# Kernel optimization log

Hardware: AMD Instinct MI355X
Metric: run time of the kernel (lower is better)

The kernel has to match this reference:

```python
import jax, jax.numpy as jnp
import numpy as np

B, LAGS, POOL, D, H, NTS = 16, 4096, 4, 512, 8, 1000
S = LAGS // POOL          # num_pools = 1024
DH = D // H               # head dim = 64


def _layernorm_dim1(x, gamma, beta, eps=1e-5):
    # torch code: mean/var over dim=1 (channel axis), unbiased var, per-position affine
    mean = jnp.mean(x, axis=1, keepdims=True)
    var = jnp.var(x, axis=1, keepdims=True, ddof=1)
    unit = (x - mean) / jnp.sqrt(eps + var)
    return gamma * unit + beta


def setup_inputs() -> dict:
    key = jax.random.key(0)
    ks = jax.random.split(key, 16)
    inp = {
        "ts": jax.random.normal(ks[0], (B, 1, LAGS), dtype=jnp.float32),
        "te": jax.random.randint(ks[1], (B, 1), 0, NTS),
        "conv_w": jax.random.normal(ks[2], (D, 1, POOL), dtype=jnp.float32) * (1.0 / POOL) ** 0.5,
        "conv_b": jax.random.normal(ks[3], (D,), dtype=jnp.float32) * 0.02,
        "pe_emb": jax.random.normal(ks[4], (S, D), dtype=jnp.float32),
        "ts_emb": jax.random.normal(ks[5], (NTS, D), dtype=jnp.float32),
        "ln1_g": jnp.ones((S,), dtype=jnp.float32),
        "ln1_b": jnp.zeros((S,), dtype=jnp.float32),
        "dense_M": jax.random.normal(ks[6], (D, D), dtype=jnp.float32) * D ** -0.5,
        "Wq": jax.random.normal(ks[7], (H, DH, D), dtype=jnp.float32) * D ** -0.5,
        "Wk": jax.random.normal(ks[8], (H, DH, D), dtype=jnp.float32) * D ** -0.5,
        "Wv": jax.random.normal(ks[9], (H, DH, D), dtype=jnp.float32) * D ** -0.5,
        "Wo": jax.random.normal(ks[10], (D, D), dtype=jnp.float32) * D ** -0.5,
        "bo": jnp.zeros((D, 1), dtype=jnp.float32),
        "ln2_g": jnp.ones((S,), dtype=jnp.float32),
        "ln2_b": jnp.zeros((S,), dtype=jnp.float32),
    }
    return inp


def _forward(ts, te, conv_w, conv_b, pe_emb, ts_emb, ln1_g, ln1_b,
             dense_M, Wq, Wk, Wv, Wo, bo, ln2_g, ln2_b):
    # Conv1d with stride == kernel_size: non-overlapping patches
    xr = ts.reshape(B, S, POOL)                                   # (B,S,P)
    conv = jnp.einsum('bsp,dp->bds', xr, conv_w[:, 0, :]) + conv_b[:, None]  # (B,D,S)
    conv = conv + pe_emb.T                                        # positional add (D,S)
    act = jax.nn.gelu(conv, approximate=False)
    n1 = _layernorm_dim1(act, ln1_g, ln1_b)
    dense = jnp.einsum('ed,bds->bes', dense_M, n1)                # Linear: M @ x
    dense = dense + ts_emb[te[:, 0]][:, :, None]                  # ts embedding (B,D,1)

    # multi-head attention, Q=K=V=dense; vectorized over heads
    Qd = jnp.einsum('hcd,bds->bhcs', Wq, dense)                   # (B,H,DH,S)
    Kd = jnp.einsum('hcd,bds->bhcs', Wk, dense)
    Vd = jnp.einsum('hcd,bds->bhcs', Wv, dense)
    scores = jnp.einsum('bhci,bhcj->bhij', Qd, Kd) / DH ** 0.5    # (B,H,S,S)
    i_idx = jnp.arange(S)
    mask = i_idx[:, None] > i_idx[None, :]                        # tril(diagonal=-1): i>j -> -inf
    scores = jnp.where(mask, -jnp.inf, scores)
    sm = jax.nn.softmax(scores, axis=2)                           # softmax over dim 1 of (S,S)
    attn = jnp.einsum('bhci,bhij->bhcj', Vd, sm)                  # V @ softmaxed
    cat = attn.reshape(B, D, S)                                   # concat heads on dim 1
    out = jnp.einsum('ed,bds->bes', Wo, cat) + bo[None]           # final linear + bias
    res = out + conv                                              # residual
    return _layernorm_dim1(res, ln2_g, ln2_b)


def reference(ts, te, conv_w, conv_b, pe_emb, ts_emb, ln1_g, ln1_b,
              dense_M, Wq, Wk, Wv, Wo, bo, ln2_g, ln2_b):
    return _forward(ts, te, conv_w, conv_b, pe_emb, ts_emb, ln1_g, ln1_b,
                    dense_M, Wq, Wk, Wv, Wo, bo, ln2_g, ln2_b)
```

## Files before the change

kernel.cpp:

```cpp
#include <hip/hip_runtime.h>
#include <hip/hip_bf16.h>

#define B_ 16
#define S_ 1024
#define D_ 512
#define H_ 8
#define DH_ 64

typedef __attribute__((ext_vector_type(8))) short bf16x8;
typedef __attribute__((ext_vector_type(4))) short bf16x4;
typedef __attribute__((ext_vector_type(4))) float f32x4;
typedef __attribute__((ext_vector_type(16))) float f32x16;

__device__ __forceinline__ short f2bf(float f) {
    __hip_bfloat16 h = __float2bfloat16(f);
    return *reinterpret_cast<short*>(&h);
}
__device__ __forceinline__ unsigned pack_bf2(float lo, float hi) {
    unsigned a = (unsigned)(unsigned short)f2bf(lo);
    unsigned b = (unsigned)(unsigned short)f2bf(hi);
    return a | (b << 16);
}
__device__ __forceinline__ void gload16(const void* g, void* l) {
    __builtin_amdgcn_global_load_lds(
        (const __attribute__((address_space(1))) unsigned int*)g,
        (__attribute__((address_space(3))) unsigned int*)l, 16, 0, 0);
}

__global__ __launch_bounds__(256) void prep_w(
    const float* __restrict__ M, const float* __restrict__ Wq,
    const float* __restrict__ Wk, const float* __restrict__ Wv,
    const float* __restrict__ Wo, __hip_bfloat16* __restrict__ wb)
{
    const int gid = blockIdx.x * 256 + threadIdx.x;
    const int e8 = gid * 8;
    const int w = e8 >> 18;
    const int off = e8 & 262143;
    const float* src = (w == 0) ? M : (w == 1) ? Wq : (w == 2) ? Wk
                      : (w == 3) ? Wv : Wo;
    const float scale = (w == 1) ? 0.18033688011112042f : 1.0f;
    const float4 f0 = *reinterpret_cast<const float4*>(src + off);
    const float4 f1 = *reinterpret_cast<const float4*>(src + off + 4);
    union { short s[8]; bf16x8 v; } r;
    r.s[0] = f2bf(f0.x * scale); r.s[1] = f2bf(f0.y * scale);
    r.s[2] = f2bf(f0.z * scale); r.s[3] = f2bf(f0.w * scale);
    r.s[4] = f2bf(f1.x * scale); r.s[5] = f2bf(f1.y * scale);
    r.s[6] = f2bf(f1.z * scale); r.s[7] = f2bf(f1.w * scale);
    *reinterpret_cast<bf16x8*>(wb + e8) = r.v;
}

__global__ __launch_bounds__(256) void k1_conv_gelu_ln(
    const float* __restrict__ ts, const float* __restrict__ conv_w,
    const float* __restrict__ conv_b, const float* __restrict__ pe,
    const float* __restrict__ g1, const float* __restrict__ b1,
    __hip_bfloat16* __restrict__ n1)
{
    const int w = threadIdx.x >> 6, lane = threadIdx.x & 63;
    const int row = blockIdx.x * 4 + w;
    const int b = row >> 10, s = row & 1023;
    const float4 x = *reinterpret_cast<const float4*>(ts + b * 4096 + s * 4);
    const int d0 = lane * 8;

    const float4 cb0 = *reinterpret_cast<const float4*>(conv_b + d0);
    const float4 cb1 = *reinterpret_cast<const float4*>(conv_b + d0 + 4);
    const float4 pe0 = *reinterpret_cast<const float4*>(pe + s * 512 + d0);
    const float4 pe1 = *reinterpret_cast<const float4*>(pe + s * 512 + d0 + 4);
    const float cbv[8] = {cb0.x, cb0.y, cb0.z, cb0.w, cb1.x, cb1.y, cb1.z, cb1.w};
    const float pev[8] = {pe0.x, pe0.y, pe0.z, pe0.w, pe1.x, pe1.y, pe1.z, pe1.w};

    float a[8];
    float sum = 0.f, sq = 0.f;
#pragma unroll
    for (int j = 0; j < 8; ++j) {
        const float4 wv = *reinterpret_cast<const float4*>(conv_w + (d0 + j) * 4);
        float v = x.x * wv.x + x.y * wv.y + x.z * wv.z + x.w * wv.w
                + cbv[j] + pev[j];
        v = 0.5f * v * (1.0f + erff(v * 0.70710678118654752f));
        a[j] = v; sum += v; sq += v * v;
    }
#pragma unroll
    for (int off = 1; off < 64; off <<= 1) {
        sum += __shfl_xor(sum, off);
        sq  += __shfl_xor(sq, off);
    }
    const float mean = sum * (1.0f / 512.0f);
    const float var  = (sq - 512.0f * mean * mean) * (1.0f / 511.0f);
    const float rstd = rsqrtf(var + 1e-5f);
    const float gg = g1[s], bb = b1[s];
    union { short sh[8]; bf16x8 v; } o;
#pragma unroll
    for (int j = 0; j < 8; ++j)
        o.sh[j] = f2bf(gg * ((a[j] - mean) * rstd) + bb);
    *reinterpret_cast<bf16x8*>(n1 + (size_t)row * 512 + d0) = o.v;
}

template<int MODE>
__global__ __launch_bounds__(256) void gemm_k(
    const __hip_bfloat16* __restrict__ A,
    const __hip_bfloat16* __restrict__ Wb,
    void* __restrict__ outp,
    const float* __restrict__ aux,
    const int* __restrict__ te)
{
    __shared__ char lA[128 * 128];
    __shared__ char lB[128 * 128];

    const int t = threadIdx.x;
    const int lane = t & 63;
    const int w = t >> 6;
    const int wm = w & 1, wn = w >> 1;
    const int Rb = blockIdx.x * 128;
    const int Nb = blockIdx.y * 128;
    const int g = lane >> 4, lr = lane & 15;
    const int lrow = lane >> 3;
    const int coff = ((lane & 7) ^ lrow) * 8;

    f32x4 acc[4][4];
#pragma unroll
    for (int i = 0; i < 4; ++i)
#pragma unroll
        for (int j = 0; j < 4; ++j) acc[i][j] = {0.f, 0.f, 0.f, 0.f};

    for (int kt = 0; kt < 8; ++kt) {
        const int k0 = kt * 64;
#pragma unroll
        for (int i = 0; i < 4; ++i) {
            const int r0 = w * 32 + i * 8;
            gload16(A + (size_t)(Rb + r0 + lrow) * 512 + k0 + coff, lA + r0 * 128);
        }
#pragma unroll
        for (int i = 0; i < 4; ++i) {
            const int r0 = w * 32 + i * 8;
            gload16(Wb + (size_t)(Nb + r0 + lrow) * 512 + k0 + coff, lB + r0 * 128);
        }
        __syncthreads();
#pragma unroll
        for (int kk = 0; kk < 2; ++kk) {
            bf16x8 af[4], bfv[4];
            const int ch = kk * 4 + g;
#pragma unroll
            for (int mt = 0; mt < 4; ++mt) {
                const int row = wm * 64 + mt * 16 + lr;
                af[mt] = *reinterpret_cast<const bf16x8*>(
                    lA + row * 128 + ((ch ^ (row & 7)) << 4));
            }
#pragma unroll
            for (int nt = 0; nt < 4; ++nt) {
                const int row = wn * 64 + nt * 16 + lr;
                bfv[nt] = *reinterpret_cast<const bf16x8*>(
                    lB + row * 128 + ((ch ^ (row & 7)) << 4));
            }
#pragma unroll
            for (int mt = 0; mt < 4; ++mt)
#pragma unroll
                for (int nt = 0; nt < 4; ++nt)
                    acc[mt][nt] = __builtin_amdgcn_mfma_f32_16x16x32_bf16(
                        af[mt], bfv[nt], acc[mt][nt], 0, 0, 0);
        }
        __syncthreads();
    }

#pragma unroll
    for (int mt = 0; mt < 4; ++mt) {
#pragma unroll
        for (int nt = 0; nt < 4; ++nt) {
#pragma unroll
            for (int r = 0; r < 4; ++r) {
                const int R = Rb + wm * 64 + mt * 16 + 4 * g + r;
                const int N = Nb + wn * 64 + nt * 16 + lr;
                float v = acc[mt][nt][r];
                if (MODE == 0) {
                    const int b = R >> 10;
                    v += aux[(size_t)te[b] * 512 + N];
                    reinterpret_cast<__hip_bfloat16*>(outp)[(size_t)R * 512 + N] =
                        __float2bfloat16(v);
                } else if (MODE == 1) {
                    const int b = R >> 10, s = R & 1023, h = N >> 6, c = N & 63;
                    reinterpret_cast<__hip_bfloat16*>(outp)
                        [(((size_t)(b * 8 + h)) * 1024 + s) * 64 + c] = __float2bfloat16(v);
                } else if (MODE == 2) {
                    const int b = R >> 10, s = R & 1023, h = N >> 6, c = N & 63;
                    reinterpret_cast<__hip_bfloat16*>(outp)
                        [(((size_t)(b * 8 + h)) * 64 + c) * 1024 + s] = __float2bfloat16(v);
                } else {
                    reinterpret_cast<float*>(outp)[(size_t)R * 512 + N] = v + aux[N];
                }
            }
        }
    }
}

__device__ __forceinline__ void write_strip(
    __hip_bfloat16* __restrict__ dstbase, const int jw0,
    const f32x16& o0, const f32x16& o1, const float lsum,
    const int l5, const int ln31)
{
    const float linv = 1.0f / lsum;
#pragma unroll
    for (int r = 0; r < 16; ++r) {
        const int jrow = (r & 3) + 8 * (r >> 2) + 4 * l5;
        const float rinv = __shfl(linv, jrow);
        __hip_bfloat16* dst = dstbase + (size_t)(jw0 + jrow) * 512;
        dst[ln31]      = __float2bfloat16(o0[r] * rinv);
        dst[32 + ln31] = __float2bfloat16(o1[r] * rinv);
    }
}

__global__ __launch_bounds__(256, 4) void attn5_k(
    const __hip_bfloat16* __restrict__ Qm,
    const __hip_bfloat16* __restrict__ Km,
    const __hip_bfloat16* __restrict__ Vt,
    __hip_bfloat16* __restrict__ cat)
{
    __shared__ char qbuf[2][4096];
    __shared__ char vbuf[2][4096];

    const int t = threadIdx.x, lane = t & 63, w = t >> 6;
    const int l5 = lane >> 5, ln31 = lane & 31;
    const int id = blockIdx.x;
    const int bh = id & 127;
    const int jb = (0x32451067u >> ((id >> 7) * 4)) & 7;
    const int b = bh >> 3, h = bh & 7;
    const int j0 = jb * 128 + w * 32;

    const __hip_bfloat16* Qh = Qm + (size_t)bh * (S_ * 64);
    const __hip_bfloat16* Kh = Km + (size_t)bh * (S_ * 64);
    const __hip_bfloat16* Vh = Vt + (size_t)bh * (64 * S_);

    bf16x8 kf[4];
#pragma unroll
    for (int kt = 0; kt < 4; ++kt)
        kf[kt] = *reinterpret_cast<const bf16x8*>(
            Kh + (size_t)(j0 + ln31) * 64 + kt * 16 + l5 * 8);

    f32x16 o0, o1;
#pragma unroll
    for (int r = 0; r < 16; ++r) { o0[r] = 0.f; o1[r] = 0.f; }
    float m = -3e38f, lsum = 0.f;

    const int last = jb * 4 + w;
    const int ntiles = jb * 4 + 4;

    const int q_row  = w * 8 + (lane >> 3);
    const int q_ch   = (lane & 7) ^ (lane >> 3);
    const int v_row  = w * 16 + (lane >> 2);
    const int v_ch   = (lane & 3) ^ ((lane >> 2) & 3) ^ ((lane >> 4) & 3);
    const __hip_bfloat16* qsrc = Qh + (size_t)q_row * 64 + q_ch * 8;
    const __hip_bfloat16* vsrc = Vh + (size_t)v_row * 1024 + v_ch * 8;

    auto stage = [&](int buf, int tile) {
        const int i0 = tile * 32;
        gload16(qsrc + (size_t)i0 * 64, &qbuf[buf][w * 1024]);
        gload16(vsrc + i0,              &vbuf[buf][w * 1024]);
    };

    stage(0, 0);
    __syncthreads();

    for (int tt = 0; tt < ntiles; ++tt) {
        const int buf = tt & 1;
        if (tt + 1 < ntiles) stage(buf ^ 1, tt + 1);
        if (tt <= last) {
            f32x16 sc;
#pragma unroll
            for (int r = 0; r < 16; ++r) sc[r] = 0.f;
            bf16x8 qf[4];
#pragma unroll
            for (int kt = 0; kt < 4; ++kt)
                qf[kt] = *reinterpret_cast<const bf16x8*>(
                    &qbuf[buf][ln31 * 128 + (((kt * 2 + l5) ^ (ln31 & 7)) << 4)]);
#pragma unroll
            for (int kt = 0; kt < 4; ++kt)
                sc = __builtin_amdgcn_mfma_f32_32x32x16_bf16(qf[kt], kf[kt], sc, 0, 0, 0);

            union u8 { bf16x4 h[2]; bf16x8 v; };
            u8 vf[2][2];
#pragma unroll
            for (int kt = 0; kt < 2; ++kt) {
#pragma unroll
                for (int dh = 0; dh < 2; ++dh) {
                    const int drow = ln31 + dh * 32;
                    const int swz = (drow & 3) ^ ((drow >> 2) & 3);
                    const int x0 = kt * 32 + 8 * l5;
#pragma unroll
                    for (int hp = 0; hp < 2; ++hp) {
                        const int x = x0 + hp * 16;
                        vf[kt][dh].h[hp] = *reinterpret_cast<const bf16x4*>(
                            &vbuf[buf][drow * 64 + (((x >> 4) ^ swz) << 4) + (x & 15)]);
                    }
                }
            }

            const bool diag = (tt == last);
            float p[16];
            float mx = -3e38f;
            if (diag) {
#pragma unroll
                for (int r = 0; r < 16; ++r) {
                    const int irow = (r & 3) + 8 * (r >> 2) + 4 * l5;
                    const float v = (irow > ln31) ? -3e38f : sc[r];
                    p[r] = v; mx = fmaxf(mx, v);
                }
            } else {
#pragma unroll
                for (int r = 0; r < 16; ++r) { p[r] = sc[r]; mx = fmaxf(mx, sc[r]); }
            }
            mx = fmaxf(mx, __shfl_xor(mx, 32));
            if (!__all(mx <= m + 8.0f)) {
                const float mn = fmaxf(m, mx);
                const float alpha = exp2f(m - mn);
                m = mn; lsum *= alpha;
#pragma unroll
                for (int r = 0; r < 16; ++r) {
                    const int jrow = (r & 3) + 8 * (r >> 2) + 4 * l5;
                    const float ar = __shfl(alpha, jrow);
                    o0[r] *= ar; o1[r] *= ar;
                }
            }
            float ps = 0.f;
#pragma unroll
            for (int r = 0; r < 16; ++r) { p[r] = exp2f(p[r] - m); ps += p[r]; }
            ps += __shfl_xor(ps, 32);
            lsum += ps;

            union { unsigned u[4]; bf16x8 v; } pa0, pa1;
            pa0.u[0] = pack_bf2(p[0],  p[1]);  pa0.u[1] = pack_bf2(p[2],  p[3]);
            pa0.u[2] = pack_bf2(p[4],  p[5]);  pa0.u[3] = pack_bf2(p[6],  p[7]);
            pa1.u[0] = pack_bf2(p[8],  p[9]);  pa1.u[1] = pack_bf2(p[10], p[11]);
            pa1.u[2] = pack_bf2(p[12], p[13]); pa1.u[3] = pack_bf2(p[14], p[15]);
            o0 = __builtin_amdgcn_mfma_f32_32x32x16_bf16(pa0.v, vf[0][0].v, o0, 0, 0, 0);
            o1 = __builtin_amdgcn_mfma_f32_32x32x16_bf16(pa0.v, vf[0][1].v, o1, 0, 0, 0);
            o0 = __builtin_amdgcn_mfma_f32_32x32x16_bf16(pa1.v, vf[1][0].v, o0, 0, 0, 0);
            o1 = __builtin_amdgcn_mfma_f32_32x32x16_bf16(pa1.v, vf[1][1].v, o1, 0, 0, 0);
        }
        __syncthreads();
    }

    __hip_bfloat16* dstbase = cat + (size_t)b * 1024 * 512 + h * 64;
    write_strip(dstbase, j0, o0, o1, lsum, l5, ln31);
}

__global__ __launch_bounds__(256) void k5_res_ln(
    const float* __restrict__ outf,
    const float* __restrict__ ts, const float* __restrict__ conv_w,
    const float* __restrict__ conv_b, const float* __restrict__ pe,
    const float* __restrict__ g2, const float* __restrict__ b2,
    float* __restrict__ out)
{
    __shared__ float tile[16 * 520];
    const int blk = blockIdx.x;
    const int b = blk >> 6, s0 = (blk & 63) * 16;
    const int t = threadIdx.x;
    const int sl = t >> 4, c = t & 15;
    const int s = s0 + sl;

    const float4 x = *reinterpret_cast<const float4*>(ts + b * 4096 + s * 4);
    float vals[32];
    float sum = 0.f, sq = 0.f;
#pragma unroll
    for (int j = 0; j < 32; ++j) {
        const int d = c + 16 * j;
        const float4 wv = *reinterpret_cast<const float4*>(conv_w + d * 4);
        const float conv = x.x * wv.x + x.y * wv.y + x.z * wv.z + x.w * wv.w
                         + conv_b[d] + pe[s * 512 + d];
        const float a = outf[(size_t)(b * 1024 + s) * 512 + d] + conv;
        vals[j] = a; sum += a; sq += a * a;
    }
#pragma unroll
    for (int off = 1; off < 16; off <<= 1) {
        sum += __shfl_xor(sum, off);
        sq  += __shfl_xor(sq, off);
    }
    const float mean = sum * (1.0f / 512.0f);
    const float var  = (sq - 512.0f * mean * mean) * (1.0f / 511.0f);
    const float rstd = rsqrtf(var + 1e-5f);
    const float gg = g2[s], bb = b2[s];
#pragma unroll
    for (int j = 0; j < 32; ++j) {
        const int d = c + 16 * j;
        tile[sl * 520 + d] = gg * ((vals[j] - mean) * rstd) + bb;
    }
    __syncthreads();
#pragma unroll
    for (int q2 = 0; q2 < 2; ++q2) {
        const int d = t + q2 * 256;
        float buf[16];
#pragma unroll
        for (int sl2 = 0; sl2 < 16; ++sl2) buf[sl2] = tile[sl2 * 520 + d];
        float4* dst = reinterpret_cast<float4*>(
            out + ((size_t)b * 512 + d) * 1024 + s0);
        dst[0] = make_float4(buf[0],  buf[1],  buf[2],  buf[3]);
        dst[1] = make_float4(buf[4],  buf[5],  buf[6],  buf[7]);
        dst[2] = make_float4(buf[8],  buf[9],  buf[10], buf[11]);
        dst[3] = make_float4(buf[12], buf[13], buf[14], buf[15]);
    }
}

extern "C" void kernel_launch(void* const* d_in, const int* in_sizes, int n_in,
                              void* d_out, int out_size, void* d_ws, size_t ws_size,
                              hipStream_t stream)
{
    const float* ts     = (const float*)d_in[0];
    const int*   te     = (const int*)d_in[1];
    const float* conv_w = (const float*)d_in[2];
    const float* conv_b = (const float*)d_in[3];
    const float* pe     = (const float*)d_in[4];
    const float* ts_emb = (const float*)d_in[5];
    const float* g1     = (const float*)d_in[6];
    const float* b1     = (const float*)d_in[7];
    const float* M      = (const float*)d_in[8];
    const float* Wq     = (const float*)d_in[9];
    const float* Wk     = (const float*)d_in[10];
    const float* Wv     = (const float*)d_in[11];
    const float* Wo     = (const float*)d_in[12];
    const float* bo     = (const float*)d_in[13];
    const float* g2     = (const float*)d_in[14];
    const float* b2     = (const float*)d_in[15];

    char* ws = (char*)d_ws;
    __hip_bfloat16* wb    = (__hip_bfloat16*)(ws);
    __hip_bfloat16* Mb    = wb;
    __hip_bfloat16* Wqb   = wb + 262144;
    __hip_bfloat16* Wkb   = wb + 2 * 262144;
    __hip_bfloat16* Wvb   = wb + 3 * 262144;
    __hip_bfloat16* Wob   = wb + 4 * 262144;
    __hip_bfloat16* n1    = (__hip_bfloat16*)(ws + ( 3ull << 20));
    __hip_bfloat16* cat   = n1;
    __hip_bfloat16* dense = (__hip_bfloat16*)(ws + (19ull << 20));
    float*          outf  = (float*)(ws + (19ull << 20));
    __hip_bfloat16* q     = (__hip_bfloat16*)(ws + (35ull << 20));
    __hip_bfloat16* k     = (__hip_bfloat16*)(ws + (51ull << 20));
    __hip_bfloat16* vT    = (__hip_bfloat16*)(ws + (67ull << 20));

    prep_w<<<640, 256, 0, stream>>>(M, Wq, Wk, Wv, Wo, wb);
    k1_conv_gelu_ln<<<4096, 256, 0, stream>>>(ts, conv_w, conv_b, pe, g1, b1, n1);
    gemm_k<0><<<dim3(128, 4), 256, 0, stream>>>(n1, Mb, dense, ts_emb, te);
    gemm_k<1><<<dim3(128, 4), 256, 0, stream>>>(dense, Wqb, q, nullptr, nullptr);
    gemm_k<1><<<dim3(128, 4), 256, 0, stream>>>(dense, Wkb, k, nullptr, nullptr);
    gemm_k<2><<<dim3(128, 4), 256, 0, stream>>>(dense, Wvb, vT, nullptr, nullptr);
    attn5_k<<<1024, 256, 0, stream>>>(q, k, vT, cat);
    gemm_k<3><<<dim3(128, 4), 256, 0, stream>>>(cat, Wob, outf, bo, nullptr);
    k5_res_ln<<<1024, 256, 0, stream>>>(outf, ts, conv_w, conv_b, pe, g2, b2,
                                        (float*)d_out);
}
```

Measured before the change: 173.4 us.

## Fold dense projection into QKV weights and fuse QKV GEMMs with double buffering

Precomputes the products Wq·M, Wk·M and Wv·M in bf16 with a small GEMM, and folds the ts_emb contribution into a per-batch QKV bias computed by a new kernel. The separate dense GEMM and three Q/K/V GEMMs are replaced by a single N=1536 GEMM that scatters into the q/k/vT layouts. The GEMM also gains double-buffered LDS staging and a launch bound of two blocks per CU. This removes one full activation GEMM pass and the dense intermediate, at the cost of extra per-call weight preprocessing and an extra bf16 rounding of the combined weights.

```diff
diff --git a/kernel.cpp b/kernel.cpp
--- a/kernel.cpp
+++ b/kernel.cpp
@@ -32,6 +32,10 @@
     const float* __restrict__ Wk, const float* __restrict__ Wv,
     const float* __restrict__ Wo, __hip_bfloat16* __restrict__ wb)
 {
+    __hip_bfloat16* wsrc = wb;
+    __hip_bfloat16* Wob  = wb + 786432;
+    __hip_bfloat16* MT   = wb + 1048576;
+
     const int gid = blockIdx.x * 256 + threadIdx.x;
     const int e8 = gid * 8;
     const int w = e8 >> 18;
@@ -41,12 +45,44 @@
     const float scale = (w == 1) ? 0.18033688011112042f : 1.0f;
     const float4 f0 = *reinterpret_cast<const float4*>(src + off);
     const float4 f1 = *reinterpret_cast<const float4*>(src + off + 4);
-    union { short s[8]; bf16x8 v; } r;
-    r.s[0] = f2bf(f0.x * scale); r.s[1] = f2bf(f0.y * scale);
-    r.s[2] = f2bf(f0.z * scale); r.s[3] = f2bf(f0.w * scale);
-    r.s[4] = f2bf(f1.x * scale); r.s[5] = f2bf(f1.y * scale);
-    r.s[6] = f2bf(f1.z * scale); r.s[7] = f2bf(f1.w * scale);
-    *reinterpret_cast<bf16x8*>(wb + e8) = r.v;
+    float fv[8] = {f0.x, f0.y, f0.z, f0.w, f1.x, f1.y, f1.z, f1.w};
+
+    if (w == 0) {
+        const int e = off >> 9, d0 = off & 511;
+#pragma unroll
+        for (int j = 0; j < 8; ++j)
+            MT[(size_t)(d0 + j) * 512 + e] = __float2bfloat16(fv[j]);
+    } else {
+        union { short s[8]; bf16x8 v; } r;
+#pragma unroll
+        for (int j = 0; j < 8; ++j) r.s[j] = f2bf(fv[j] * scale);
+        __hip_bfloat16* dst = (w == 4) ? (Wob + off) : (wsrc + (w - 1) * 262144 + off);
+        *reinterpret_cast<bf16x8*>(dst) = r.v;
+    }
+}
+
+__global__ __launch_bounds__(256) void bias_k(
+    const float* __restrict__ Wq, const float* __restrict__ Wk,
+    const float* __restrict__ Wv, const float* __restrict__ ts_emb,
+    const int* __restrict__ te, float* __restrict__ qkvbias)
+{
+    const int blk = blockIdx.x;
+    const int w = blk >> 4, b = blk & 15;
+    const float* W = (w == 0) ? Wq : (w == 1) ? Wk : Wv;
+    const float scale = (w == 0) ? 0.18033688011112042f : 1.0f;
+    const float* e = ts_emb + (size_t)te[b] * 512;
+#pragma unroll
+    for (int rep = 0; rep < 2; ++rep) {
+        const int n = threadIdx.x + rep * 256;
+        const float* wr = W + (size_t)n * 512;
+        float s = 0.f;
+        for (int d = 0; d < 512; d += 4) {
+            const float4 a = *reinterpret_cast<const float4*>(wr + d);
+            const float4 bb = *reinterpret_cast<const float4*>(e + d);
+            s += a.x * bb.x + a.y * bb.y + a.z * bb.z + a.w * bb.w;
+        }
+        qkvbias[(size_t)(w * 16 + b) * 512 + n] = s * scale;
+    }
 }
 
 __global__ __launch_bounds__(256) void k1_conv_gelu_ln(
@@ -95,15 +131,14 @@
 }
 
 template<int MODE>
-__global__ __launch_bounds__(256) void gemm_k(
+__global__ __launch_bounds__(256, 2) void gemm_k(
     const __hip_bfloat16* __restrict__ A,
     const __hip_bfloat16* __restrict__ Wb,
     void* __restrict__ outp,
-    const float* __restrict__ aux,
-    const int* __restrict__ te)
-{
-    __shared__ char lA[128 * 128];
-    __shared__ char lB[128 * 128];
+    const float* __restrict__ aux)
+{
+    __shared__ char lA[2][128 * 128];
+    __shared__ char lB[2][128 * 128];
 
     const int t = threadIdx.x;
     const int lane = t & 63;
@@ -115,25 +150,34 @@
     const int lrow = lane >> 3;
     const int coff = ((lane & 7) ^ lrow) * 8;
 
+    const __hip_bfloat16* asrc = A  + (size_t)(Rb + lrow) * 512 + coff;
+    const __hip_bfloat16* bsrc = Wb + (size_t)(Nb + lrow) * 512 + coff;
+
     f32x4 acc[4][4];
 #pragma unroll
     for (int i = 0; i < 4; ++i)
 #pragma unroll
         for (int j = 0; j < 4; ++j) acc[i][j] = {0.f, 0.f, 0.f, 0.f};
 
-    for (int kt = 0; kt < 8; ++kt) {
-        const int k0 = kt * 64;
+    auto stage = [&](int buf, int k0) {
 #pragma unroll
         for (int i = 0; i < 4; ++i) {
             const int r0 = w * 32 + i * 8;
-            gload16(A + (size_t)(Rb + r0 + lrow) * 512 + k0 + coff, lA + r0 * 128);
+            gload16(asrc + (size_t)r0 * 512 + k0, &lA[buf][r0 * 128]);
         }
 #pragma unroll
         for (int i = 0; i < 4; ++i) {
             const int r0 = w * 32 + i * 8;
-            gload16(Wb + (size_t)(Nb + r0 + lrow) * 512 + k0 + coff, lB + r0 * 128);
-        }
-        __syncthreads();
+            gload16(bsrc + (size_t)r0 * 512 + k0, &lB[buf][r0 * 128]);
+        }
+    };
+
+    stage(0, 0);
+    __syncthreads();
+
+    for (int kt = 0; kt < 8; ++kt) {
+        const int buf = kt & 1;
+        if (kt < 7) stage(buf ^ 1, (kt + 1) * 64);
 #pragma unroll
         for (int kk = 0; kk < 2; ++kk) {
             bf16x8 af[4], bfv[4];
@@ -142,13 +186,13 @@
             for (int mt = 0; mt < 4; ++mt) {
                 const int row = wm * 64 + mt * 16 + lr;
                 af[mt] = *reinterpret_cast<const bf16x8*>(
-                    lA + row * 128 + ((ch ^ (row & 7)) << 4));
+                    &lA[buf][row * 128 + ((ch ^ (row & 7)) << 4)]);
             }
 #pragma unroll
             for (int nt = 0; nt < 4; ++nt) {
                 const int row = wn * 64 + nt * 16 + lr;
                 bfv[nt] = *reinterpret_cast<const bf16x8*>(
-                    lB + row * 128 + ((ch ^ (row & 7)) << 4));
+                    &lB[buf][row * 128 + ((ch ^ (row & 7)) << 4)]);
             }
 #pragma unroll
             for (int mt = 0; mt < 4; ++mt)
@@ -160,6 +204,7 @@
         __syncthreads();
     }
 
+    const int w3 = Nb >> 9;
 #pragma unroll
     for (int mt = 0; mt < 4; ++mt) {
 #pragma unroll
@@ -169,19 +214,21 @@
                 const int R = Rb + wm * 64 + mt * 16 + 4 * g + r;
                 const int N = Nb + wn * 64 + nt * 16 + lr;
                 float v = acc[mt][nt][r];
-                if (MODE == 0) {
-                    const int b = R >> 10;
-                    v += aux[(size_t)te[b] * 512 + N];
+                if (MODE == 5) {
+                    const int Nl = N & 511;
+                    const int b = R >> 10, s = R & 1023, h = Nl >> 6, c = Nl & 63;
+                    v += aux[(size_t)(w3 * 16 + b) * 512 + Nl];
+                    __hip_bfloat16* base =
+                        reinterpret_cast<__hip_bfloat16*>(outp) + (size_t)w3 * 8388608;
+                    if (w3 == 2)
+                        base[(((size_t)(b * 8 + h)) * 64 + c) * 1024 + s] =
+                            __float2bfloat16(v);
+                    else
+                        base[(((size_t)(b * 8 + h)) * 1024 + s) * 64 + c] =
+                            __float2bfloat16(v);
+                } else if (MODE == 6) {
                     reinterpret_cast<__hip_bfloat16*>(outp)[(size_t)R * 512 + N] =
                         __float2bfloat16(v);
-                } else if (MODE == 1) {
-                    const int b = R >> 10, s = R & 1023, h = N >> 6, c = N & 63;
-                    reinterpret_cast<__hip_bfloat16*>(outp)
-                        [(((size_t)(b * 8 + h)) * 1024 + s) * 64 + c] = __float2bfloat16(v);
-                } else if (MODE == 2) {
-                    const int b = R >> 10, s = R & 1023, h = N >> 6, c = N & 63;
-                    reinterpret_cast<__hip_bfloat16*>(outp)
-                        [(((size_t)(b * 8 + h)) * 64 + c) * 1024 + s] = __float2bfloat16(v);
                 } else {
                     reinterpret_cast<float*>(outp)[(size_t)R * 512 + N] = v + aux[N];
                 }
@@ -418,28 +465,26 @@
     const float* b2     = (const float*)d_in[15];
 
     char* ws = (char*)d_ws;
-    __hip_bfloat16* wb    = (__hip_bfloat16*)(ws);
-    __hip_bfloat16* Mb    = wb;
-    __hip_bfloat16* Wqb   = wb + 262144;
-    __hip_bfloat16* Wkb   = wb + 2 * 262144;
-    __hip_bfloat16* Wvb   = wb + 3 * 262144;
-    __hip_bfloat16* Wob   = wb + 4 * 262144;
-    __hip_bfloat16* n1    = (__hip_bfloat16*)(ws + ( 3ull << 20));
-    __hip_bfloat16* cat   = n1;
-    __hip_bfloat16* dense = (__hip_bfloat16*)(ws + (19ull << 20));
-    float*          outf  = (float*)(ws + (19ull << 20));
-    __hip_bfloat16* q     = (__hip_bfloat16*)(ws + (35ull << 20));
-    __hip_bfloat16* k     = (__hip_bfloat16*)(ws + (51ull << 20));
-    __hip_bfloat16* vT    = (__hip_bfloat16*)(ws + (67ull << 20));
+    __hip_bfloat16* wb     = (__hip_bfloat16*)(ws);
+    __hip_bfloat16* wsrc   = wb;
+    __hip_bfloat16* Wob    = wb + 786432;
+    __hip_bfloat16* MT     = wb + 1048576;
+    __hip_bfloat16* Wqkvp  = (__hip_bfloat16*)(ws + (2688ull << 10));
+    float*          qkvbias= (float*)(ws + (4608ull << 10));
+    __hip_bfloat16* n1     = (__hip_bfloat16*)(ws + ( 6ull << 20));
+    __hip_bfloat16* cat    = n1;
+    __hip_bfloat16* q      = (__hip_bfloat16*)(ws + (22ull << 20));
+    __hip_bfloat16* k      = (__hip_bfloat16*)(ws + (38ull << 20));
+    __hip_bfloat16* vT     = (__hip_bfloat16*)(ws + (54ull << 20));
+    float*          outf   = (float*)(ws + (22ull << 20));
 
     prep_w<<<640, 256, 0, stream>>>(M, Wq, Wk, Wv, Wo, wb);
+    bias_k<<<48, 256, 0, stream>>>(Wq, Wk, Wv, ts_emb, te, qkvbias);
+    gemm_k<6><<<dim3(12, 4), 256, 0, stream>>>(wsrc, MT, Wqkvp, nullptr);
     k1_conv_gelu_ln<<<4096, 256, 0, stream>>>(ts, conv_w, conv_b, pe, g1, b1, n1);
-    gemm_k<0><<<dim3(128, 4), 256, 0, stream>>>(n1, Mb, dense, ts_emb, te);
-    gemm_k<1><<<dim3(128, 4), 256, 0, stream>>>(dense, Wqb, q, nullptr, nullptr);
-    gemm_k<1><<<dim3(128, 4), 256, 0, stream>>>(dense, Wkb, k, nullptr, nullptr);
-    gemm_k<2><<<dim3(128, 4), 256, 0, stream>>>(dense, Wvb, vT, nullptr, nullptr);
+    gemm_k<5><<<dim3(128, 12), 256, 0, stream>>>(n1, Wqkvp, q, qkvbias);
     attn5_k<<<1024, 256, 0, stream>>>(q, k, vT, cat);
-    gemm_k<3><<<dim3(128, 4), 256, 0, stream>>>(cat, Wob, outf, bo, nullptr);
+    gemm_k<3><<<dim3(128, 4), 256, 0, stream>>>(cat, Wob, outf, bo);
     k5_res_ln<<<1024, 256, 0, stream>>>(outf, ts, conv_w, conv_b, pe, g2, b2,
                                         (float*)d_out);
 }
```

Result: slower. 198.1 us (+14.2%).
